# Kernel optimization log

Hardware: AMD Instinct MI355X
Metric: run time of the kernel (lower is better)

The kernel has to match this reference:

```python
import jax, jax.numpy as jnp
import numpy as np

B, S, HID = 2, 2048, 2048
H, HKV, D = 16, 8, 128
CHUNK = 512
THETA = 1000000.0
NEG = -1e9


def setup_inputs() -> dict:
    key = jax.random.key(0)
    ks = jax.random.split(key, 10)
    hidden_states = jax.random.normal(ks[0], (B, S, HID), dtype=jnp.float32)
    # additive causal mask (0 on/below diagonal, -1e9 above)
    tri = jnp.tril(jnp.ones((S, S), dtype=bool))
    attention_mask = jnp.where(tri, 0.0, NEG).astype(jnp.float32)
    attention_mask = jnp.broadcast_to(attention_mask[None, None], (B, 1, S, S))
    w = 0.02
    Wq = jax.random.normal(ks[1], (HID, H * D), dtype=jnp.float32) * w
    bq = jax.random.normal(ks[2], (H * D,), dtype=jnp.float32) * w
    Wk = jax.random.normal(ks[3], (HID, HKV * D), dtype=jnp.float32) * w
    bk = jax.random.normal(ks[4], (HKV * D,), dtype=jnp.float32) * w
    Wv = jax.random.normal(ks[5], (HID, HKV * D), dtype=jnp.float32) * w
    bv = jax.random.normal(ks[6], (HKV * D,), dtype=jnp.float32) * w
    Wo = jax.random.normal(ks[7], (H * D, HID), dtype=jnp.float32) * w
    bo = jax.random.normal(ks[8], (HID,), dtype=jnp.float32) * w
    return {"hidden_states": hidden_states, "attention_mask": attention_mask,
            "Wq": Wq, "bq": bq, "Wk": Wk, "bk": bk, "Wv": Wv, "bv": bv,
            "Wo": Wo, "bo": bo}


def _rope_tables(seq_len, dim):
    inv_freq = 1.0 / (THETA ** (jnp.arange(0, dim, 2, dtype=jnp.float32) / dim))
    pos = jnp.arange(seq_len, dtype=jnp.float32)
    freqs = pos[:, None] * inv_freq[None, :]          # [S, D/2]
    emb = jnp.concatenate([freqs, freqs], axis=-1)    # [S, D]
    return jnp.cos(emb)[None, None], jnp.sin(emb)[None, None]  # [1,1,S,D]


def _rotate_half(x):
    x1, x2 = jnp.split(x, 2, axis=-1)
    return jnp.concatenate([-x2, x1], axis=-1)


def _attn_forward(hidden_states, attention_mask, Wq, bq, Wk, bk, Wv, bv, Wo, bo):
    bsz, s, _ = hidden_states.shape
    q = (hidden_states @ Wq + bq).reshape(bsz, s, H, D).transpose(0, 2, 1, 3)
    k = (hidden_states @ Wk + bk).reshape(bsz, s, HKV, D).transpose(0, 2, 1, 3)
    v = (hidden_states @ Wv + bv).reshape(bsz, s, HKV, D).transpose(0, 2, 1, 3)
    cos, sin = _rope_tables(s, D)
    q = q * cos + _rotate_half(q) * sin
    k = k * cos + _rotate_half(k) * sin
    n_rep = H // HKV
    k = jnp.repeat(k, n_rep, axis=1)  # repeat_kv
    v = jnp.repeat(v, n_rep, axis=1)
    scale = 1.0 / jnp.sqrt(jnp.float32(D))
    nq, nk = s // CHUNK, s // CHUNK
    Qc = q.reshape(bsz, H, nq, CHUNK, D)
    Kc = jnp.moveaxis(k.reshape(bsz, H, nk, CHUNK, D), 2, 0)   # [nk,B,H,Ck,D]
    Vc = jnp.moveaxis(v.reshape(bsz, H, nk, CHUNK, D), 2, 0)
    Mc = jnp.moveaxis(attention_mask.reshape(bsz, 1, nq, CHUNK, nk, CHUNK), 4, 0)  # [nk,B,1,nq,Cq,Ck]

    def step(carry, xs):
        o, m, d = carry
        k_seg, v_seg, m_seg = xs
        # scores: [B,H,nq,Cq,Ck]
        sc = jnp.einsum('bhqcd,bhkd->bhqck', Qc, k_seg) * scale + m_seg
        new_m = jnp.maximum(m, sc.max(axis=-1, keepdims=True))
        e = jnp.exp(sc - new_m)
        sums = e.sum(axis=-1, keepdims=True)
        prev = jnp.exp(m - new_m)          # NOTE: uses running max, as in source
        d_new = prev + sums
        o = (o * prev + jnp.einsum('bhqck,bhkd->bhqcd', e, v_seg)) / d_new
        return (o, new_m, d_new), None

    o0 = jnp.zeros((bsz, H, nq, CHUNK, D), dtype=jnp.float32)
    m0 = jnp.full((bsz, H, nq, CHUNK, 1), -jnp.inf, dtype=jnp.float32)
    d0 = jnp.ones((bsz, H, nq, CHUNK, 1), dtype=jnp.float32)
    (o, m, d), _ = jax.lax.scan(step, (o0, m0, d0), (Kc, Vc, Mc))
    # final rescale: attn_output * exp(max - logsumexp) == o / d_last (source math)
    o = o / d
    attn = o.reshape(bsz, H, s, D).transpose(0, 2, 1, 3).reshape(bsz, s, H * D)
    return attn @ Wo + bo


def reference(hidden_states, attention_mask, Wq, bq, Wk, bk, Wv, bv, Wo, bo):
    return _attn_forward(hidden_states, attention_mask, Wq, bq, Wk, bk, Wv, bv, Wo, bo)
```

## Files before the change

kernel.cpp:

```cpp
#include <hip/hip_runtime.h>
#include <hip/hip_bf16.h>


typedef __attribute__((ext_vector_type(8))) short s8v;
typedef __attribute__((ext_vector_type(4))) float f4v;
typedef __attribute__((ext_vector_type(4))) unsigned int u32x4;

#define MFMA16(a, b, c) __builtin_amdgcn_mfma_f32_16x16x32_bf16((a), (b), (c), 0, 0, 0)

typedef unsigned short u16;
typedef const __attribute__((address_space(1))) unsigned int* gas_p;
typedef __attribute__((address_space(3))) unsigned int* las_p;

template <bool B> struct BoolC { static constexpr bool value = B; };

__device__ __forceinline__ void gl_lds16(const void* g, void* l) {
    __builtin_amdgcn_global_load_lds((gas_p)g, (las_p)l, 16, 0, 0);
}

__device__ __forceinline__ u16 f2b(float f) {
    __hip_bfloat16 h = __float2bfloat16(f);
    return *reinterpret_cast<u16*>(&h);
}
__device__ __forceinline__ float b2f(u16 u) {
    __hip_bfloat16 h;
    *reinterpret_cast<u16*>(&h) = u;
    return __bfloat162float(h);
}

__device__ __forceinline__ void qswap(unsigned int& a, unsigned int& b) {
#if __has_builtin(__builtin_amdgcn_permlane32_swap) && __has_builtin(__builtin_amdgcn_permlane16_swap)
    typedef __attribute__((ext_vector_type(2))) unsigned int u32x2;
    u32x2 r1 = __builtin_amdgcn_permlane32_swap(a, b, false, false);
    u32x2 r2 = __builtin_amdgcn_permlane16_swap(r1[0], r1[1], false, false);
    a = r2[0]; b = r2[1];
#else
    asm volatile("v_permlane32_swap_b32 %0, %1\n\t"
                 "s_nop 0\n\t"
                 "v_permlane16_swap_b32 %0, %1\n\t"
                 "s_nop 0"
                 : "+v"(a), "+v"(b));
#endif
}

__device__ const unsigned char qt_tab[40] = {
    4, 5, 6, 7,
    8, 8, 9, 9, 10, 10, 11, 11,
    12, 12, 12, 13, 13, 13, 14, 14, 14, 15, 15, 15,
    3, 7, 11, 15, 2, 6, 10, 14, 1, 5, 9, 13, 0, 4, 8, 12};
__device__ const unsigned char c_tab[40] = {
    0, 0, 0, 0,
    0, 1, 0, 1, 0, 1, 0, 1,
    0, 1, 2, 0, 1, 2, 0, 1, 2, 0, 1, 2,
    0, 1, 2, 3, 0, 1, 2, 3, 0, 1, 2, 3, 0, 1, 2, 3};

__device__ __forceinline__ int uoff40(int qt, int c) {
    int qc = qt >> 2;
    if (c < qc) {
        if (qt < 8) return qt - 4;
        if (qt < 12) return 4 + ((qt - 8) << 1) + c;
        return 12 + (qt - 12) * 3 + c;
    }
    return 24 + ((3 - (qt & 3)) << 2) + qc;
}

__global__ __launch_bounds__(256) void k_cast_hs(const float* __restrict__ src,
                                                 u16* __restrict__ dst) {
    int i = blockIdx.x * 256 + threadIdx.x;
    float4 v = reinterpret_cast<const float4*>(src)[i];
    alignas(8) u16 t[4] = {f2b(v.x), f2b(v.y), f2b(v.z), f2b(v.w)};
    reinterpret_cast<uint2*>(dst)[i] = *reinterpret_cast<uint2*>(t);
}

__global__ __launch_bounds__(256) void k_transpose_w(
    const float* __restrict__ Wq, const float* __restrict__ Wk,
    const float* __restrict__ Wv, const float* __restrict__ Wo,
    u16* __restrict__ wt_all, u16* __restrict__ wo_t) {
    int id = blockIdx.x;
    const float* W; u16* dst; int N, nbase;
    if (id < 4096)      { W = Wq; dst = wt_all; N = 2048; nbase = 0; }
    else if (id < 6144) { W = Wk; dst = wt_all; N = 1024; nbase = 2048; id -= 4096; }
    else if (id < 8192) { W = Wv; dst = wt_all; N = 1024; nbase = 3072; id -= 6144; }
    else                { W = Wo; dst = wo_t;  N = 2048; nbase = 0;    id -= 8192; }
    int tiles_n = N >> 5;
    int k0 = (id / tiles_n) << 5, n0 = (id % tiles_n) << 5;
    __shared__ float t[32][33];
    int tid = threadIdx.x;
    {
        int row = tid >> 3, c4 = (tid & 7) << 2;
        float4 v = *reinterpret_cast<const float4*>(&W[(size_t)(k0 + row) * N + n0 + c4]);
        t[row][c4 + 0] = v.x; t[row][c4 + 1] = v.y;
        t[row][c4 + 2] = v.z; t[row][c4 + 3] = v.w;
    }
    __syncthreads();
    {
        int n = tid >> 3, kq = (tid & 7) << 2;
        alignas(8) u16 p[4];
#pragma unroll
        for (int j = 0; j < 4; j++) p[j] = f2b(t[kq + j][n]);
        *reinterpret_cast<uint2*>(&dst[(size_t)(nbase + n0 + n) * 2048 + k0 + kq]) =
            *reinterpret_cast<uint2*>(p);
    }
}

__global__ __launch_bounds__(512) void k_gemm256(
    const u16* __restrict__ A, const u16* __restrict__ Bt,
    const float* __restrict__ bq, const float* __restrict__ bk,
    const float* __restrict__ bv, u16* __restrict__ out,
    int M, int N, int K) {
    __shared__ alignas(16) u16 As[2][256][64];
    __shared__ alignas(16) u16 Bs[2][256][64];
    int tid = threadIdx.x;
    int wave = tid >> 6, lane = tid & 63, quad = lane >> 4, l16 = lane & 15;
    int gx = gridDim.x;
    int nb = gx * gridDim.y;
    int wg = blockIdx.y * gx + blockIdx.x;
    int lsw = (wg & 7) * (nb >> 3) + (wg >> 3);
    int tm = lsw / gx, tn = lsw % gx;
    int m0 = tm << 8, n0 = tn << 8;
    int wm = (wave >> 2) << 7;
    int wn = (wave & 3) << 6;
    f4v zero = {0.f, 0.f, 0.f, 0.f};
    f4v acc[8][4];
#pragma unroll
    for (int a = 0; a < 8; a++)
#pragma unroll
        for (int b = 0; b < 4; b++) acc[a][b] = zero;
    int sr = tid >> 3, sg = (tid & 7) ^ (sr & 7);
    const u16* gA = A + (size_t)(m0 + sr) * K + (sg << 3);
    const u16* gB = Bt + (size_t)(n0 + sr) * K + (sg << 3);
    auto stageA = [&](int t) {
        char* d = (char*)&As[t & 1][0][0];
        int k0 = t << 6;
#pragma unroll
        for (int j = 0; j < 4; j++)
            gl_lds16(gA + (size_t)(j << 6) * K + k0, d + (j << 13) + tid * 16);
    };
    auto stageB = [&](int t) {
        char* d = (char*)&Bs[t & 1][0][0];
        int k0 = t << 6;
#pragma unroll
        for (int j = 0; j < 4; j++)
            gl_lds16(gB + (size_t)(j << 6) * K + k0, d + (j << 13) + tid * 16);
    };
    int NT = K >> 6;
    stageA(0); stageB(0); stageB(1);
    for (int t = 0; t < NT; t++) {
        int cur = t & 1;
        if (t + 1 < NT)
            asm volatile("s_waitcnt vmcnt(4)" ::: "memory");
        else
            asm volatile("s_waitcnt vmcnt(0)" ::: "memory");
        __builtin_amdgcn_sched_barrier(0);
        __builtin_amdgcn_s_barrier();
        __builtin_amdgcn_sched_barrier(0);
        if (t + 1 < NT) stageA(t + 1);
        s8v bf[2][4], af[8];
#pragma unroll
        for (int kk = 0; kk < 2; kk++)
#pragma unroll
            for (int ni = 0; ni < 4; ni++)
                bf[kk][ni] = *reinterpret_cast<const s8v*>(
                    &Bs[cur][wn + ni * 16 + l16][((((kk << 2) | quad) ^ (l16 & 7)) << 3)]);
#pragma unroll
        for (int mi = 0; mi < 8; mi++)
            af[mi] = *reinterpret_cast<const s8v*>(
                &As[cur][wm + mi * 16 + l16][((quad ^ (l16 & 7)) << 3)]);
        __builtin_amdgcn_s_setprio(1);
#pragma unroll
        for (int mi = 0; mi < 8; mi++)
#pragma unroll
            for (int ni = 0; ni < 4; ni++)
                acc[mi][ni] = MFMA16(af[mi], bf[0][ni], acc[mi][ni]);
        __builtin_amdgcn_s_setprio(0);
        asm volatile("s_waitcnt lgkmcnt(0)" ::: "memory");
        __builtin_amdgcn_sched_barrier(0);
        __builtin_amdgcn_s_barrier();
        __builtin_amdgcn_sched_barrier(0);
        if (t + 2 < NT) stageB(t + 2);
#pragma unroll
        for (int mi = 0; mi < 8; mi++)
            af[mi] = *reinterpret_cast<const s8v*>(
                &As[cur][wm + mi * 16 + l16][(((4 | quad) ^ (l16 & 7)) << 3)]);
        __builtin_amdgcn_s_setprio(1);
#pragma unroll
        for (int mi = 0; mi < 8; mi++)
#pragma unroll
            for (int ni = 0; ni < 4; ni++)
                acc[mi][ni] = MFMA16(af[mi], bf[1][ni], acc[mi][ni]);
        __builtin_amdgcn_s_setprio(0);
        asm volatile("s_waitcnt lgkmcnt(0)" ::: "memory");
        __builtin_amdgcn_sched_barrier(0);
    }
#pragma unroll
    for (int ni = 0; ni < 4; ni++) {
        int n = n0 + wn + ni * 16 + l16;
        float bsv = (n < 2048) ? bq[n] : (n < 3072) ? bk[n - 2048] : bv[n - 3072];
#pragma unroll
        for (int mi = 0; mi < 8; mi++)
#pragma unroll
            for (int r = 0; r < 4; r++)
                out[(size_t)(m0 + wm + mi * 16 + (quad << 2) + r) * N + n] =
                    f2b(acc[mi][ni][r] + bsv);
    }
}

__global__ __launch_bounds__(256) void k_gemm(
    const u16* __restrict__ A, const u16* __restrict__ Bt,
    const float* __restrict__ bias, void* __restrict__ out,
    int M, int N, int K, int out_f32) {
    __shared__ alignas(16) u16 As[2][128][64];
    __shared__ alignas(16) u16 Bs[2][128][64];
    int tid = threadIdx.x;
    int wave = tid >> 6, lane = tid & 63, quad = lane >> 4, l16 = lane & 15;
    int nwg = gridDim.x * gridDim.y;
    int wg = blockIdx.y * gridDim.x + blockIdx.x;
    int l = (wg & 7) * (nwg >> 3) + (wg >> 3);
    int t4 = l >> 4, a4 = l & 15;
    int tn4 = gridDim.x >> 2;
    int tm = t4 / tn4, tn = t4 % tn4;
    int m0 = ((tm << 2) + (a4 >> 2)) << 7;
    int n0 = ((tn << 2) + (a4 & 3)) << 7;
    int wm = (wave >> 1) << 6, wn = (wave & 1) << 6;
    f4v zero = {0.f, 0.f, 0.f, 0.f};
    f4v acc[4][4];
#pragma unroll
    for (int a = 0; a < 4; a++)
#pragma unroll
        for (int b = 0; b < 4; b++) acc[a][b] = zero;
    int r0 = tid >> 3;
    int gsw = (tid & 7) ^ (r0 & 7);
    const u16* gA = A + (size_t)(m0 + r0) * K + (gsw << 3);
    const u16* gB = Bt + (size_t)(n0 + r0) * K + (gsw << 3);
    auto stage = [&](int k0, int buf) {
#pragma unroll
        for (int i = 0; i < 4; i++) {
            gl_lds16(gA + (size_t)(i << 5) * K + k0,
                     (char*)&As[buf][0][0] + (i << 12) + tid * 16);
            gl_lds16(gB + (size_t)(i << 5) * K + k0,
                     (char*)&Bs[buf][0][0] + (i << 12) + tid * 16);
        }
    };
    int NT = K >> 6;
    stage(0, 0);
    stage(64, 1);
    for (int t = 0; t < NT; t++) {
        int cur = t & 1;
        if (t + 1 < NT)
            asm volatile("s_waitcnt vmcnt(8)" ::: "memory");
        else
            asm volatile("s_waitcnt vmcnt(0)" ::: "memory");
        __builtin_amdgcn_sched_barrier(0);
        __builtin_amdgcn_s_barrier();
        __builtin_amdgcn_sched_barrier(0);
#pragma unroll
        for (int ks = 0; ks < 2; ks++) {
            int rg = (((ks << 2) | quad) ^ (l16 & 7)) << 3;
            s8v af[4], bf_[4];
#pragma unroll
            for (int mi = 0; mi < 4; mi++)
                af[mi] = *reinterpret_cast<const s8v*>(&As[cur][wm + mi * 16 + l16][rg]);
#pragma unroll
            for (int ni = 0; ni < 4; ni++)
                bf_[ni] = *reinterpret_cast<const s8v*>(&Bs[cur][wn + ni * 16 + l16][rg]);
#pragma unroll
            for (int mi = 0; mi < 4; mi++)
#pragma unroll
                for (int ni = 0; ni < 4; ni++)
                    acc[mi][ni] = MFMA16(af[mi], bf_[ni], acc[mi][ni]);
        }
        asm volatile("s_waitcnt lgkmcnt(0)" ::: "memory");
        __builtin_amdgcn_sched_barrier(0);
        __builtin_amdgcn_s_barrier();
        __builtin_amdgcn_sched_barrier(0);
        if (t + 2 < NT) stage((t + 2) << 6, cur);
    }
    if (!out_f32) {
        u16* cs = &As[0][0][0];
#pragma unroll
        for (int ni = 0; ni < 4; ni++) {
            int col = wn + ni * 16 + l16;
            float bsv = bias[n0 + col];
#pragma unroll
            for (int mi = 0; mi < 4; mi++)
#pragma unroll
                for (int r = 0; r < 4; r++) {
                    int row = wm + mi * 16 + (quad << 2) + r;
                    cs[row * 128 + ((((col >> 3) ^ (row & 7)) << 3) | (col & 7))] =
                        f2b(acc[mi][ni][r] + bsv);
                }
        }
        __syncthreads();
        int row = tid >> 1, c8 = (tid & 1) << 3;
        u16* dst = (u16*)out + (size_t)(m0 + row) * N + n0 + (c8 << 3);
#pragma unroll
        for (int j = 0; j < 8; j++) {
            int g = (c8 + j) ^ (row & 7);
            *reinterpret_cast<uint4*>(dst + j * 8) =
                *reinterpret_cast<const uint4*>(&cs[row * 128 + g * 8]);
        }
    } else {
        float* cf = (float*)&As[0][0][0];
#pragma unroll
        for (int p = 0; p < 2; p++) {
            __syncthreads();
            if ((wm >> 6) == p) {
#pragma unroll
                for (int ni = 0; ni < 4; ni++) {
                    int col = wn + ni * 16 + l16;
                    float bsv = bias[n0 + col];
#pragma unroll
                    for (int mi = 0; mi < 4; mi++)
#pragma unroll
                        for (int r = 0; r < 4; r++) {
                            int lr = (wm - (p << 6)) + mi * 16 + (quad << 2) + r;
                            cf[lr * 128 + ((((col >> 2) ^ (lr & 7)) << 2) | (col & 3))] =
                                acc[mi][ni][r] + bsv;
                        }
                }
            }
            __syncthreads();
            int row = tid >> 2, g0 = (tid & 3) << 3;
            float* dst = (float*)out + (size_t)(m0 + (p << 6) + row) * N + n0 + (g0 << 2);
#pragma unroll
            for (int j = 0; j < 8; j++) {
                int g = (g0 + j) ^ (row & 7);
                *reinterpret_cast<uint4*>(dst + j * 4) =
                    *reinterpret_cast<const uint4*>(&cf[row * 128 + g * 4]);
            }
        }
    }
}

__global__ __launch_bounds__(256) void k_rope(const u16* __restrict__ qkv,
                                              u16* __restrict__ qr,
                                              u16* __restrict__ kr) {
    const float qscale = 0.08838834764831845f * 1.44269504088896340f;
    int row = blockIdx.x;
    int b = row >> 11, s = row & 2047;
    const u16* src = qkv + (size_t)row * 4096;
    __shared__ float lcs[64], lsn[64];
    int tid = threadIdx.x;
    if (tid < 64) {
        float fr = (float)s * exp2f((float)tid * -0.31143075889569023f);
        lcs[tid] = cosf(fr);
        lsn[tid] = sinf(fr);
    }
    __syncthreads();
    for (int u = tid; u < 1536; u += 256) {
        int hh, i;
        const u16* sp;
        u16* dp;
        float sc;
        if (u < 1024) {
            hh = u >> 6; i = u & 63;
            sp = src + hh * 128;
            dp = qr + ((size_t)(b * 16 + hh) * 2048 + s) * 128;
            sc = qscale;
        } else {
            int u2 = u - 1024;
            hh = u2 >> 6; i = u2 & 63;
            sp = src + 2048 + hh * 128;
            dp = kr + ((size_t)(b * 8 + hh) * 2048 + s) * 128;
            sc = 1.f;
        }
        float x1 = b2f(sp[i]);
        float x2 = b2f(sp[i + 64]);
        float cs = lcs[i], sn = lsn[i];
        dp[i]      = f2b((x1 * cs - x2 * sn) * sc);
        dp[i + 64] = f2b((x2 * cs + x1 * sn) * sc);
    }
}

__global__ __launch_bounds__(256) void k_vtrans(const u16* __restrict__ qkv,
                                                u16* __restrict__ vt) {
    int bkv = blockIdx.z, b = bkv >> 3, kv = bkv & 7;
    int s0 = blockIdx.x << 6, d0 = blockIdx.y << 5;
    __shared__ alignas(16) u16 t[32][72];
    int tid = threadIdx.x, c = tid & 31, rr = tid >> 5;
#pragma unroll
    for (int i = 0; i < 8; i++) {
        int s = s0 + rr + i * 8;
        t[c][rr + i * 8] = qkv[(size_t)(b * 2048 + s) * 4096 + 3072 + kv * 128 + d0 + c];
    }
    __syncthreads();
    int dd = tid >> 3, sc8 = (tid & 7) << 3;
    *reinterpret_cast<uint4*>(&vt[((size_t)(b * 8 + kv) * 128 + d0 + dd) * 2048 + s0 + sc8]) =
        *reinterpret_cast<const uint4*>(&t[dd][sc8]);
}

__global__ __launch_bounds__(256, 3) void k_attn_part(const u16* __restrict__ qr,
                                                      const u16* __restrict__ kr,
                                                      const u16* __restrict__ vt,
                                                      u16* __restrict__ PVp,
                                                      float* __restrict__ scp) {
    const float NINF = -__builtin_inff();
    __shared__ alignas(16) u16 Ks[2][64 * 128];
    __shared__ alignas(16) u16 Vs[128 * 64];

    int tid = threadIdx.x;
    int wv = tid >> 6, lane = tid & 63, quad = lane >> 4, l16 = lane & 15;
    int x = blockIdx.x, h = blockIdx.y, b = blockIdx.z, kvh = h >> 1;
    int qt = qt_tab[x], c = c_tab[x], qc = qt >> 2;
    bool diag = (c == qc);
    int m3 = qt & 3;
    int nt = diag ? ((m3 + 1) << 1) : 8;
    int kbase = c << 9;
    const u16* Qp = qr + ((size_t)(b * 16 + h) * 2048 + qt * 128 + wv * 32) * 128;
    const u16* Kp = kr + ((size_t)(b * 8 + kvh) * 2048) * 128;
    const u16* Vp = vt + ((size_t)(b * 8 + kvh) * 128) * 2048;

    s8v qf0[4], qf1[4];
#pragma unroll
    for (int sl = 0; sl < 4; sl++) {
        qf0[sl] = *reinterpret_cast<const s8v*>(&Qp[l16 * 128 + sl * 32 + (quad << 3)]);
        qf1[sl] = *reinterpret_cast<const s8v*>(&Qp[(16 + l16) * 128 + sl * 32 + (quad << 3)]);
    }
    s8v ones;
#pragma unroll
    for (int i = 0; i < 8; i++) ones[i] = (short)0x3F80;
    s8v pzero;
#pragma unroll
    for (int i = 0; i < 8; i++) pzero[i] = (short)0;

    int krow = tid >> 4, kg = (tid & 15) ^ krow;
    int vd = tid >> 3, vg = (tid & 7) ^ (vd & 7);
    auto stageK = [&](int t) {
        int kbt = kbase + (t << 6);
        const u16* kgp = Kp + (size_t)(kbt + krow) * 128 + (kg << 3);
        char* kd = (char*)&Ks[t & 1][0];
#pragma unroll
        for (int i = 0; i < 4; i++)
            gl_lds16(kgp + (size_t)(i << 4) * 128, kd + (i << 12) + tid * 16);
    };
    auto stageV = [&](int t) {
        int kbt = kbase + (t << 6);
        const u16* vgp = Vp + (size_t)vd * 2048 + kbt + (vg << 3);
        char* vdst = (char*)&Vs[0];
#pragma unroll
        for (int i = 0; i < 4; i++)
            gl_lds16(vgp + (size_t)(i << 5) * 2048, vdst + (i << 12) + tid * 16);
    };

    auto pack = [&](const f4v& s, bool tri, bool act, float& tmx,
                    unsigned int& wlo, unsigned int& whi) {
        if (!act) { wlo = 0u; whi = 0u; return; }
        float e[4];
#pragma unroll
        for (int r = 0; r < 4; r++) {
            float v = s[r];
            if (tri && ((quad << 2) + r > l16)) v = NINF;
            tmx = fmaxf(tmx, v);
            e[r] = __builtin_amdgcn_exp2f(v);
        }
        wlo = (unsigned int)f2b(e[0]) | ((unsigned int)f2b(e[1]) << 16);
        whi = (unsigned int)f2b(e[2]) | ((unsigned int)f2b(e[3]) << 16);
    };

    f4v zero = {0.f, 0.f, 0.f, 0.f};
    f4v u0[8], u1[8], sums0 = zero, sums1 = zero;
#pragma unroll
    for (int ni = 0; ni < 8; ni++) { u0[ni] = zero; u1[ni] = zero; }
    float tmx0 = NINF, tmx1 = NINF;
    int qg0 = wv << 1, qg1 = (wv << 1) + 1;

    auto run = [&](auto diagc) {
        constexpr bool DIAG = decltype(diagc)::value;
        stageK(0);
        for (int t = 0; t < nt; t++) {
            __syncthreads();
            stageV(t);
            if (t + 1 < nt) stageK(t + 1);
            const char* Kbuf = (const char*)&Ks[t & 1][0];
            int kgb = DIAG ? ((t << 2) - (m3 << 3)) : 0;
            s8v pa0s[2], pa1s[2];
            bool act0[2], act1[2];
#pragma unroll
            for (int s2 = 0; s2 < 2; s2++) {
                int kgA = kgb + (s2 << 1), kgB = kgA + 1;
                bool skip = DIAG && (kgA > qg1);
                bool a0 = !DIAG || (kgA <= qg0);
                bool b0 = !DIAG || (kgB <= qg0);
                bool b1 = !DIAG || (kgB <= qg1);
                act1[s2] = !skip;
                act0[s2] = !skip && a0;
                if (skip) { pa0s[s2] = pzero; pa1s[s2] = pzero; continue; }
                f4v sA0 = zero, sA1 = zero, sB0 = zero, sB1 = zero;
#pragma unroll
                for (int sl = 0; sl < 4; sl++) {
                    s8v kf = *reinterpret_cast<const s8v*>(
                        Kbuf + (((s2 << 1) << 4) + l16) * 256 +
                        ((((sl << 2) + quad) ^ l16) << 4));
                    if (a0) sA0 = MFMA16(kf, qf0[sl], sA0);
                    sA1 = MFMA16(kf, qf1[sl], sA1);
                }
                if (b1) {
#pragma unroll
                    for (int sl = 0; sl < 4; sl++) {
                        s8v kf = *reinterpret_cast<const s8v*>(
                            Kbuf + ((((s2 << 1) | 1) << 4) + l16) * 256 +
                            ((((sl << 2) + quad) ^ l16) << 4));
                        if (b0) sB0 = MFMA16(kf, qf0[sl], sB0);
                        sB1 = MFMA16(kf, qf1[sl], sB1);
                    }
                }
                unsigned int A0w, A1w, B0w, B1w;
                pack(sA1, DIAG && (kgA == qg1), true, tmx1, A0w, A1w);
                pack(sB1, DIAG && (kgB == qg1), b1, tmx1, B0w, B1w);
                qswap(A0w, B0w); qswap(A1w, B1w);
                u32x4 pw1 = {A0w, A1w, B0w, B1w};
                pa1s[s2] = __builtin_bit_cast(s8v, pw1);
                if (a0) {
                    unsigned int C0w, C1w, D0w, D1w;
                    pack(sA0, DIAG && (kgA == qg0), true, tmx0, C0w, C1w);
                    pack(sB0, DIAG && (kgB == qg0), b0, tmx0, D0w, D1w);
                    qswap(C0w, D0w); qswap(C1w, D1w);
                    u32x4 pw0 = {C0w, C1w, D0w, D1w};
                    pa0s[s2] = __builtin_bit_cast(s8v, pw0);
                } else {
                    pa0s[s2] = pa1s[s2];
                }
            }
            __syncthreads();
#pragma unroll
            for (int s2 = 0; s2 < 2; s2++) {
                if (DIAG && !act1[s2]) continue;
                bool a0 = !DIAG || act0[s2];
                if (a0) sums0 = MFMA16(pa0s[s2], ones, sums0);
                sums1 = MFMA16(pa1s[s2], ones, sums1);
#pragma unroll
                for (int ni = 0; ni < 8; ni++) {
                    s8v vf = *reinterpret_cast<const s8v*>(
                        (const char*)&Vs[0] + ((ni << 4) + l16) * 128 +
                        ((((s2 << 2) + quad) ^ (l16 & 7)) << 4));
                    if (a0) u0[ni] = MFMA16(pa0s[s2], vf, u0[ni]);
                    u1[ni] = MFMA16(pa1s[s2], vf, u1[ni]);
                }
            }
        }
    };
    if (diag) run(BoolC<true>{}); else run(BoolC<false>{});

    tmx0 = fmaxf(tmx0, __shfl_xor(tmx0, 16));
    tmx0 = fmaxf(tmx0, __shfl_xor(tmx0, 32));
    tmx1 = fmaxf(tmx1, __shfl_xor(tmx1, 16));
    tmx1 = fmaxf(tmx1, __shfl_xor(tmx1, 32));
    float m0[4], m1[4], resc0[4], resc1[4];
#pragma unroll
    for (int r = 0; r < 4; r++) {
        m0[r] = __shfl(tmx0, (quad << 2) + r);
        m1[r] = __shfl(tmx1, (quad << 2) + r);
        resc0[r] = __builtin_amdgcn_exp2f(-m0[r]);
        resc1[r] = __builtin_amdgcn_exp2f(-m1[r]);
    }
    int slot = (b * 16 + h) * 40 + x;
    u16* pvdst = PVp + (size_t)slot * 16384;
    int row0 = wv * 32 + (quad << 2);
#pragma unroll
    for (int ni = 0; ni < 8; ni++)
#pragma unroll
        for (int r = 0; r < 4; r++) {
            pvdst[(row0 + r) * 128 + ni * 16 + l16] = f2b(u0[ni][r] * resc0[r]);
            pvdst[(row0 + 16 + r) * 128 + ni * 16 + l16] = f2b(u1[ni][r] * resc1[r]);
        }
    if (l16 == 0) {
        float* scd = scp + (size_t)slot * 256 + row0;
#pragma unroll
        for (int r = 0; r < 4; r++) {
            scd[r] = m0[r] * 0.6931471805599453f;
            scd[16 + r] = m1[r] * 0.6931471805599453f;
            scd[128 + r] = sums0[r] * resc0[r];
            scd[144 + r] = sums1[r] * resc1[r];
        }
    }
}

__global__ __launch_bounds__(256) void k_attn_comb(const u16* __restrict__ PVp,
                                                   const float* __restrict__ scp,
                                                   u16* __restrict__ attnb) {
    int qt64 = blockIdx.x, h = blockIdx.y, b = blockIdx.z;
    int qt = qt64 >> 1, qc = qt >> 2;
    int tid = threadIdx.x;
    int row = ((qt64 & 1) << 6) + (tid >> 2), d0 = (tid & 3) << 5;
    int bh = b * 16 + h;
    float o[32];
#pragma unroll
    for (int i = 0; i < 32; i++) o[i] = 0.f;
    float mprev = -__builtin_inff(), dlast = 1.f;
    for (int cc = 0; cc <= qc; cc++) {
        int slot = bh * 40 + uoff40(qt, cc);
        float ch = scp[(size_t)slot * 256 + row];
        float sh = scp[(size_t)slot * 256 + 128 + row];
        float mnew = fmaxf(mprev, ch);
        float p = __expf(mprev - mnew);
        float lam = __expf(ch - mnew);
        float dd = p + lam * sh;
        float inv = 1.f / dd;
        const u16* pv = PVp + (size_t)slot * 16384 + row * 128 + d0;
#pragma unroll
        for (int k = 0; k < 4; k++) {
            s8v v8 = *reinterpret_cast<const s8v*>(pv + (k << 3));
#pragma unroll
            for (int j = 0; j < 8; j++) {
                int i = (k << 3) + j;
                o[i] = (o[i] * p + lam * b2f((u16)v8[j])) * inv;
            }
        }
        mprev = mnew;
        dlast = dd;
    }
    if (qc == 3) {
        float inv = 1.f / dlast;
#pragma unroll
        for (int i = 0; i < 32; i++) o[i] *= inv;
    }
    alignas(16) u16 ob[32];
#pragma unroll
    for (int i = 0; i < 32; i++) ob[i] = f2b(o[i]);
    u16* dst = attnb + (size_t)(b * 2048 + qt * 128 + row) * 2048 + h * 128 + d0;
#pragma unroll
    for (int k = 0; k < 4; k++)
        reinterpret_cast<uint4*>(dst)[k] = reinterpret_cast<const uint4*>(ob)[k];
}

extern "C" void kernel_launch(void* const* d_in, const int* in_sizes, int n_in,
                              void* d_out, int out_size, void* d_ws, size_t ws_size,
                              hipStream_t stream) {
    (void)in_sizes; (void)n_in; (void)out_size; (void)ws_size;
    const float* hs = (const float*)d_in[0];
    const float* Wq = (const float*)d_in[2];
    const float* bq = (const float*)d_in[3];
    const float* Wk = (const float*)d_in[4];
    const float* bk = (const float*)d_in[5];
    const float* Wv = (const float*)d_in[6];
    const float* bv = (const float*)d_in[7];
    const float* Wo = (const float*)d_in[8];
    const float* bo = (const float*)d_in[9];

    char* ws = (char*)d_ws;
    u16* hsb      = (u16*)(ws);
    u16* qr       = hsb;
    u16* attnb    = hsb;
    u16* wt_all   = (u16*)(ws + (16u << 20));
    u16* kr       = wt_all;
    u16* vt       = (u16*)(ws + (24u << 20));
    u16* wo_t     = (u16*)(ws + (32u << 20));
    u16* qkv      = (u16*)(ws + (40u << 20) + 65536);
    u16* PVp      = qkv;
    float* scp    = (float*)(ws + (40u << 20) + 65536 + 41943040u);

    k_cast_hs<<<8192, 256, 0, stream>>>(hs, hsb);
    k_transpose_w<<<12288, 256, 0, stream>>>(Wq, Wk, Wv, Wo, wt_all, wo_t);
    k_gemm256<<<dim3(16, 16), 512, 0, stream>>>(hsb, wt_all, bq, bk, bv, qkv,
                                                4096, 4096, 2048);
    k_rope<<<4096, 256, 0, stream>>>(qkv, qr, kr);
    k_vtrans<<<dim3(32, 4, 16), 256, 0, stream>>>(qkv, vt);
    k_attn_part<<<dim3(40, 16, 2), 256, 0, stream>>>(qr, kr, vt, PVp, scp);
    k_attn_comb<<<dim3(32, 16, 2), 256, 0, stream>>>(PVp, scp, attnb);
    k_gemm<<<dim3(16, 32), 256, 0, stream>>>(attnb, wo_t, bo, d_out,
                                             4096, 2048, 2048, 1);
}
```

Baseline: 361.5 us.

## Interleave QKV GEMM main loop into four sub-phases with split prefetches

Restructures the fused QKV projection GEMM's K-loop into four quarter-phases, each handling half of the M fragments and half of the K slice. Each phase issues a small LDS fragment load, a barrier, and its MFMA block. Global-to-LDS prefetches for the next tile are split into halves and spread across the phases, so memory traffic overlaps compute more evenly. B for the next tile is now prefetched one step ahead instead of two, which trades earlier latency hiding for more frequent barriers and lower register pressure from fewer live fragments.

```diff
diff --git a/kernel.cpp b/kernel.cpp
--- a/kernel.cpp
+++ b/kernel.cpp
@@ -129,68 +129,97 @@
     int sr = tid >> 3, sg = (tid & 7) ^ (sr & 7);
     const u16* gA = A + (size_t)(m0 + sr) * K + (sg << 3);
     const u16* gB = Bt + (size_t)(n0 + sr) * K + (sg << 3);
-    auto stageA = [&](int t) {
+    auto stageA_h = [&](int t, int h) {
         char* d = (char*)&As[t & 1][0][0];
         int k0 = t << 6;
 #pragma unroll
-        for (int j = 0; j < 4; j++)
+        for (int j = (h << 1); j < (h << 1) + 2; j++)
             gl_lds16(gA + (size_t)(j << 6) * K + k0, d + (j << 13) + tid * 16);
     };
-    auto stageB = [&](int t) {
+    auto stageB_h = [&](int t, int h) {
         char* d = (char*)&Bs[t & 1][0][0];
         int k0 = t << 6;
 #pragma unroll
-        for (int j = 0; j < 4; j++)
+        for (int j = (h << 1); j < (h << 1) + 2; j++)
             gl_lds16(gB + (size_t)(j << 6) * K + k0, d + (j << 13) + tid * 16);
     };
     int NT = K >> 6;
-    stageA(0); stageB(0); stageB(1);
+    stageA_h(0, 0); stageA_h(0, 1); stageB_h(0, 0); stageB_h(0, 1);
+    int cA0 = (quad ^ (l16 & 7)) << 3;
+    int cA1 = ((4 | quad) ^ (l16 & 7)) << 3;
     for (int t = 0; t < NT; t++) {
         int cur = t & 1;
-        if (t + 1 < NT)
-            asm volatile("s_waitcnt vmcnt(4)" ::: "memory");
-        else
-            asm volatile("s_waitcnt vmcnt(0)" ::: "memory");
-        __builtin_amdgcn_sched_barrier(0);
-        __builtin_amdgcn_s_barrier();
-        __builtin_amdgcn_sched_barrier(0);
-        if (t + 1 < NT) stageA(t + 1);
-        s8v bf[2][4], af[8];
-#pragma unroll
-        for (int kk = 0; kk < 2; kk++)
+        bool pf = (t + 1 < NT);
+        s8v bf0[4], bf1[4], af[4];
+        if (pf) { stageB_h(t + 1, 0); stageB_h(t + 1, 1); }
+        if (pf) asm volatile("s_waitcnt vmcnt(4)" ::: "memory");
+        else    asm volatile("s_waitcnt vmcnt(0)" ::: "memory");
+        __builtin_amdgcn_sched_barrier(0);
+        __builtin_amdgcn_s_barrier();
+        __builtin_amdgcn_sched_barrier(0);
+#pragma unroll
+        for (int ni = 0; ni < 4; ni++)
+            bf0[ni] = *reinterpret_cast<const s8v*>(&Bs[cur][wn + ni * 16 + l16][cA0]);
+#pragma unroll
+        for (int mi = 0; mi < 4; mi++)
+            af[mi] = *reinterpret_cast<const s8v*>(&As[cur][wm + mi * 16 + l16][cA0]);
+        asm volatile("s_waitcnt lgkmcnt(0)" ::: "memory");
+        __builtin_amdgcn_sched_barrier(0);
+        __builtin_amdgcn_s_setprio(1);
+#pragma unroll
+        for (int mi = 0; mi < 4; mi++)
 #pragma unroll
             for (int ni = 0; ni < 4; ni++)
-                bf[kk][ni] = *reinterpret_cast<const s8v*>(
-                    &Bs[cur][wn + ni * 16 + l16][((((kk << 2) | quad) ^ (l16 & 7)) << 3)]);
-#pragma unroll
-        for (int mi = 0; mi < 8; mi++)
-            af[mi] = *reinterpret_cast<const s8v*>(
-                &As[cur][wm + mi * 16 + l16][((quad ^ (l16 & 7)) << 3)]);
+                acc[mi][ni] = MFMA16(af[mi], bf0[ni], acc[mi][ni]);
+        __builtin_amdgcn_s_setprio(0);
+        __builtin_amdgcn_s_barrier();
+#pragma unroll
+        for (int mi = 0; mi < 4; mi++)
+            af[mi] = *reinterpret_cast<const s8v*>(&As[cur][wm + (mi + 4) * 16 + l16][cA0]);
+        if (pf) stageA_h(t + 1, 0);
+        __builtin_amdgcn_s_barrier();
+        asm volatile("s_waitcnt lgkmcnt(0)" ::: "memory");
+        __builtin_amdgcn_sched_barrier(0);
         __builtin_amdgcn_s_setprio(1);
 #pragma unroll
-        for (int mi = 0; mi < 8; mi++)
+        for (int mi = 0; mi < 4; mi++)
 #pragma unroll
             for (int ni = 0; ni < 4; ni++)
-                acc[mi][ni] = MFMA16(af[mi], bf[0][ni], acc[mi][ni]);
+                acc[mi + 4][ni] = MFMA16(af[mi], bf0[ni], acc[mi + 4][ni]);
         __builtin_amdgcn_s_setprio(0);
+        __builtin_amdgcn_s_barrier();
+#pragma unroll
+        for (int ni = 0; ni < 4; ni++)
+            bf1[ni] = *reinterpret_cast<const s8v*>(&Bs[cur][wn + ni * 16 + l16][cA1]);
+#pragma unroll
+        for (int mi = 0; mi < 4; mi++)
+            af[mi] = *reinterpret_cast<const s8v*>(&As[cur][wm + mi * 16 + l16][cA1]);
+        if (pf) stageA_h(t + 1, 1);
+        __builtin_amdgcn_s_barrier();
         asm volatile("s_waitcnt lgkmcnt(0)" ::: "memory");
         __builtin_amdgcn_sched_barrier(0);
-        __builtin_amdgcn_s_barrier();
-        __builtin_amdgcn_sched_barrier(0);
-        if (t + 2 < NT) stageB(t + 2);
-#pragma unroll
-        for (int mi = 0; mi < 8; mi++)
-            af[mi] = *reinterpret_cast<const s8v*>(
-                &As[cur][wm + mi * 16 + l16][(((4 | quad) ^ (l16 & 7)) << 3)]);
         __builtin_amdgcn_s_setprio(1);
 #pragma unroll
-        for (int mi = 0; mi < 8; mi++)
+        for (int mi = 0; mi < 4; mi++)
 #pragma unroll
             for (int ni = 0; ni < 4; ni++)
-                acc[mi][ni] = MFMA16(af[mi], bf[1][ni], acc[mi][ni]);
+                acc[mi][ni] = MFMA16(af[mi], bf1[ni], acc[mi][ni]);
         __builtin_amdgcn_s_setprio(0);
+        __builtin_amdgcn_s_barrier();
+#pragma unroll
+        for (int mi = 0; mi < 4; mi++)
+            af[mi] = *reinterpret_cast<const s8v*>(&As[cur][wm + (mi + 4) * 16 + l16][cA1]);
+        __builtin_amdgcn_s_barrier();
         asm volatile("s_waitcnt lgkmcnt(0)" ::: "memory");
         __builtin_amdgcn_sched_barrier(0);
+        __builtin_amdgcn_s_setprio(1);
+#pragma unroll
+        for (int mi = 0; mi < 4; mi++)
+#pragma unroll
+            for (int ni = 0; ni < 4; ni++)
+                acc[mi + 4][ni] = MFMA16(af[mi], bf1[ni], acc[mi + 4][ni]);
+        __builtin_amdgcn_s_setprio(0);
+        __builtin_amdgcn_s_barrier();
     }
 #pragma unroll
     for (int ni = 0; ni < 4; ni++) {
```

Result: no change. 362.6 us (+0.3%).
